# Kernel tuning notes

Hardware: AMD Instinct MI355X
Metric: run time of the kernel (lower is better)

The kernel has to match this reference:

```python
import jax, jax.numpy as jnp
import numpy as np

N = 8192          # number of nodes
DIN = 512         # in_features
DOUT = 256        # out_features
P_EDGE = 0.004    # ~32 avg degree
NEG_INF = -9e15   # matches the torch module's -9000000000000000.0 mask value


def setup_inputs() -> dict:
    key = jax.random.key(0)
    ks = jax.random.split(key, 7)
    x = jax.random.normal(ks[0], (N, DIN), dtype=jnp.float32)
    # binary adjacency, Bernoulli(P_EDGE)
    adj = (jax.random.uniform(ks[1], (N, N)) < P_EDGE).astype(jnp.float32)
    W1 = jax.random.normal(ks[2], (DIN, DOUT), dtype=jnp.float32) * 0.05
    b1 = jnp.zeros((DOUT,), dtype=jnp.float32)
    a1_w = jax.random.normal(ks[3], (DOUT,), dtype=jnp.float32) * 0.05
    a1_b = jnp.zeros((), dtype=jnp.float32)
    a2_w = jax.random.normal(ks[4], (DOUT,), dtype=jnp.float32) * 0.05
    a2_b = jnp.zeros((), dtype=jnp.float32)
    return {"x": x, "adj": adj, "W1": W1, "b1": b1,
            "a1_w": a1_w, "a1_b": a1_b, "a2_w": a2_w, "a2_b": a2_b}


def reference(x, adj, W1, b1, a1_w, a1_b, a2_w, a2_b):
    # h = linear1(elu(x))                       [n, DOUT]
    h = jnp.matmul(jax.nn.elu(x), W1) + b1
    # per-node scalar scores g1 (source/col) and g2 (dest/row)
    g1 = h @ a1_w + a1_b                       # [n]
    g2 = h @ a2_w + a2_b                       # [n]
    # kron trick collapses to: scores[i,j] = adj[i,j] * (g2[i] + g1[j])
    scores = adj * (g2[:, None] + g1[None, :])  # [n, n]
    e = jax.nn.leaky_relu(scores, negative_slope=0.2)
    attention = jax.nn.softmax(jnp.where(adj > 0, e, NEG_INF), axis=1)
    # untied=False path: weighted aggregation of h (dropout p=0 is identity)
    return attention @ h
```

## Files before the change

### kernel.cpp

```cpp
#include <hip/hip_runtime.h>
#include <hip/hip_bf16.h>
#include <cstdint>
#include <cstddef>

#define N_NODES 8192
#define DIN 512
#define DOUT 256
#define CAP 512

typedef short bf16x8 __attribute__((ext_vector_type(8)));
typedef float f32x4 __attribute__((ext_vector_type(4)));
typedef unsigned int u32x4 __attribute__((ext_vector_type(4)));

__device__ __forceinline__ float bf2f(unsigned short u) {
    union { unsigned int ui; float f; } v; v.ui = ((unsigned int)u) << 16; return v.f;
}
__device__ __forceinline__ unsigned short f2bf(float f) {
    union { float f; unsigned int u; } v; v.f = f;
    unsigned int u = v.u;
    return (unsigned short)((u + 0x7fffu + ((u >> 16) & 1u)) >> 16);
}
__device__ __forceinline__ float elu1(float v) { return v > 0.f ? v : (expf(v) - 1.f); }

__global__ __launch_bounds__(256) void gemm_h_kernel(
    const float* __restrict__ x, const float* __restrict__ W1,
    const float* __restrict__ b1, unsigned short* __restrict__ h)
{
    const int tid = threadIdx.x;
    const int wave = tid >> 6, lane = tid & 63;
    const int quad = lane >> 4, r16 = lane & 15;
    const int m0 = (blockIdx.x >> 2) * 64;
    const int col = (blockIdx.x & 3) * 64 + wave * 16 + r16;

    f32x4 acc[4] = {{0.f,0.f,0.f,0.f},{0.f,0.f,0.f,0.f},{0.f,0.f,0.f,0.f},{0.f,0.f,0.f,0.f}};

    for (int k0 = 0; k0 < DIN; k0 += 32) {
        const int kbase = k0 + quad * 8;
        bf16x8 bfr;
        #pragma unroll
        for (int j = 0; j < 8; ++j)
            bfr[j] = (short)f2bf(W1[(size_t)(kbase + j) * DOUT + col]);
        #pragma unroll
        for (int r = 0; r < 4; ++r) {
            const float* xrow = x + (size_t)(m0 + r * 16 + r16) * DIN;
            float4 f0 = *(const float4*)(xrow + kbase);
            float4 f1 = *(const float4*)(xrow + kbase + 4);
            bf16x8 af;
            af[0] = (short)f2bf(elu1(f0.x)); af[1] = (short)f2bf(elu1(f0.y));
            af[2] = (short)f2bf(elu1(f0.z)); af[3] = (short)f2bf(elu1(f0.w));
            af[4] = (short)f2bf(elu1(f1.x)); af[5] = (short)f2bf(elu1(f1.y));
            af[6] = (short)f2bf(elu1(f1.z)); af[7] = (short)f2bf(elu1(f1.w));
            acc[r] = __builtin_amdgcn_mfma_f32_16x16x32_bf16(af, bfr, acc[r], 0, 0, 0);
        }
    }
    const float bias = b1[col];
    #pragma unroll
    for (int r = 0; r < 4; ++r)
        #pragma unroll
        for (int rr = 0; rr < 4; ++rr)
            h[(size_t)(m0 + r * 16 + quad * 4 + rr) * DOUT + col] = f2bf(acc[r][rr] + bias);
}

__global__ __launch_bounds__(256) void g12_kernel(
    const unsigned short* __restrict__ h,
    const float* __restrict__ a1w, const float* __restrict__ a1b,
    const float* __restrict__ a2w, const float* __restrict__ a2b,
    float* __restrict__ g1, float* __restrict__ g2)
{
    const int tid = threadIdx.x;
    const int wave = tid >> 6, lane = tid & 63;
    const int i = blockIdx.x * 4 + wave;
    const int d0 = lane * 4;
    ushort4 hv = *(const ushort4*)(h + (size_t)i * DOUT + d0);
    float4 w1 = *(const float4*)(a1w + d0);
    float4 w2 = *(const float4*)(a2w + d0);
    float h0 = bf2f(hv.x), h1 = bf2f(hv.y), h2 = bf2f(hv.z), h3 = bf2f(hv.w);
    float s1 = h0*w1.x + h1*w1.y + h2*w1.z + h3*w1.w;
    float s2 = h0*w2.x + h1*w2.y + h2*w2.z + h3*w2.w;
    #pragma unroll
    for (int off = 32; off > 0; off >>= 1) {
        s1 += __shfl_xor(s1, off, 64);
        s2 += __shfl_xor(s2, off, 64);
    }
    if (lane == 0) {
        g1[i] = s1 + a1b[0];
        g2[i] = s2 + a2b[0];
    }
}

__global__ __launch_bounds__(256) void scan_kernel(
    const float* __restrict__ adj, const float* __restrict__ g1,
    const float* __restrict__ g2,
    int* __restrict__ ej, float* __restrict__ evg, int* __restrict__ cnts)
{
    __shared__ int   eidx[CAP];
    __shared__ float ev[CAP];
    __shared__ int   cnt;

    const int tid = threadIdx.x;
    const int i = blockIdx.x;
    if (tid == 0) cnt = 0;
    __syncthreads();

    const float g2i = g2[i];
    const float* arow = adj + (size_t)i * N_NODES;

    u32x4 raws[8];
    #pragma unroll
    for (int c = 0; c < 8; ++c)
        raws[c] = __builtin_nontemporal_load((const u32x4*)(arow + c * 1024 + tid * 4));

    #pragma unroll
    for (int c = 0; c < 8; ++c) {
        u32x4 raw = raws[c];
        if (raw.x | raw.y | raw.z | raw.w) {
            unsigned int wv[4] = {raw.x, raw.y, raw.z, raw.w};
            #pragma unroll
            for (int q = 0; q < 4; ++q) {
                if (wv[q]) {
                    int j = c * 1024 + tid * 4 + q;
                    union { unsigned int u; float f; } av; av.u = wv[q];
                    float s = av.f * (g2i + g1[j]);
                    float lr = s > 0.f ? s : 0.2f * s;
                    int pos = atomicAdd(&cnt, 1);
                    if (pos < CAP) { eidx[pos] = j; ev[pos] = lr; }
                }
            }
        }
    }
    __syncthreads();
    const int K = cnt < CAP ? cnt : CAP;
    for (int k = tid; k < K; k += 256) {
        ej[(size_t)i * CAP + k]  = eidx[k];
        evg[(size_t)i * CAP + k] = ev[k];
    }
    if (tid == 0) cnts[i] = K;
}

__global__ __launch_bounds__(256) void finish_kernel(
    const int* __restrict__ ej, const float* __restrict__ evg,
    const int* __restrict__ cnts, const unsigned short* __restrict__ h,
    float* __restrict__ out)
{
    __shared__ int   jbuf[CAP];
    __shared__ float pbuf[CAP];
    __shared__ float sinv;

    const int tid = threadIdx.x;
    const int i = blockIdx.x;
    const int K = cnts[i];

    if (K == 0) {
        float acc = 0.f;
        for (int j = 0; j < N_NODES; ++j) acc += bf2f(h[(size_t)j * DOUT + tid]);
        out[(size_t)i * DOUT + tid] = acc / (float)N_NODES;
        return;
    }

    for (int k = tid; k < K; k += 256) {
        jbuf[k] = ej[(size_t)i * CAP + k];
        pbuf[k] = evg[(size_t)i * CAP + k];
    }
    __syncthreads();

    if (tid < 64) {
        const int lane = tid;
        float mloc = -1e30f;
        for (int k = lane; k < K; k += 64) mloc = fmaxf(mloc, pbuf[k]);
        #pragma unroll
        for (int off = 32; off > 0; off >>= 1) mloc = fmaxf(mloc, __shfl_xor(mloc, off, 64));
        float sloc = 0.f;
        for (int k = lane; k < K; k += 64) { float p = expf(pbuf[k] - mloc); pbuf[k] = p; sloc += p; }
        #pragma unroll
        for (int off = 32; off > 0; off >>= 1) sloc += __shfl_xor(sloc, off, 64);
        if (lane == 0) sinv = 1.f / sloc;
    }
    __syncthreads();
    const float inv = sinv;

    float acc = 0.f;
    int k = 0;
    for (; k + 4 <= K; k += 4) {
        float p0 = pbuf[k],   p1 = pbuf[k+1], p2 = pbuf[k+2], p3 = pbuf[k+3];
        int   j0 = jbuf[k],   j1 = jbuf[k+1], j2 = jbuf[k+2], j3 = jbuf[k+3];
        float v0 = bf2f(h[(size_t)j0 * DOUT + tid]);
        float v1 = bf2f(h[(size_t)j1 * DOUT + tid]);
        float v2 = bf2f(h[(size_t)j2 * DOUT + tid]);
        float v3 = bf2f(h[(size_t)j3 * DOUT + tid]);
        acc += p0 * v0 + p1 * v1 + p2 * v2 + p3 * v3;
    }
    for (; k < K; ++k) acc += pbuf[k] * bf2f(h[(size_t)jbuf[k] * DOUT + tid]);
    out[(size_t)i * DOUT + tid] = acc * inv;
}

extern "C" void kernel_launch(void* const* d_in, const int* in_sizes, int n_in,
                              void* d_out, int out_size, void* d_ws, size_t ws_size,
                              hipStream_t stream) {
    const float* x   = (const float*)d_in[0];
    const float* adj = (const float*)d_in[1];
    const float* W1  = (const float*)d_in[2];
    const float* b1  = (const float*)d_in[3];
    const float* a1w = (const float*)d_in[4];
    const float* a1b = (const float*)d_in[5];
    const float* a2w = (const float*)d_in[6];
    const float* a2b = (const float*)d_in[7];

    char* w = (char*)d_ws;
    float* g1 = (float*)w;                                   w += (size_t)N_NODES * 4;
    float* g2 = (float*)w;                                   w += (size_t)N_NODES * 4;
    unsigned short* h = (unsigned short*)w;                  w += (size_t)N_NODES * DOUT * 2;
    int* ej = (int*)w;                                       w += (size_t)N_NODES * CAP * 4;
    float* evg = (float*)w;                                  w += (size_t)N_NODES * CAP * 4;
    int* cnts = (int*)w;
    float* out = (float*)d_out;

    hipLaunchKernelGGL(gemm_h_kernel,  dim3(512),  dim3(256), 0, stream, x, W1, b1, h);
    hipLaunchKernelGGL(g12_kernel,     dim3(2048), dim3(256), 0, stream, h, a1w, a1b, a2w, a2b, g1, g2);
    hipLaunchKernelGGL(scan_kernel,    dim3(8192), dim3(256), 0, stream, adj, g1, g2, ej, evg, cnts);
    hipLaunchKernelGGL(finish_kernel,  dim3(8192), dim3(256), 0, stream, ej, evg, cnts, h, out);
}
```

Baseline: 427.0 us.

## Flatten adjacency scan into grid-stride pass with global atomics; compute scores in finish

The scan no longer assigns one block per row. It now sweeps the whole adjacency matrix with a grid-stride loop of coalesced 16-byte loads, and appends column indices per row through global atomics on a per-row counter. A new kernel zeroes those counters first. Edge scores are no longer computed and stored in the scan; finish recomputes leaky_relu(g2[i]+g1[j]) from the gathered indices, which drops the evg buffer traffic and the shared-memory staging and block syncs in the scan. The change assumes adjacency values are exactly 1 and makes edge order, and so summation order, nondeterministic.

```diff
diff --git a/kernel.cpp b/kernel.cpp
--- a/kernel.cpp
+++ b/kernel.cpp
@@ -7,6 +7,7 @@
 #define DIN 512
 #define DOUT 256
 #define CAP 512
+#define NCHUNK (N_NODES * N_NODES / 4)
 
 typedef short bf16x8 __attribute__((ext_vector_type(8)));
 typedef float f32x4 __attribute__((ext_vector_type(4)));
@@ -21,6 +22,10 @@
     return (unsigned short)((u + 0x7fffu + ((u >> 16) & 1u)) >> 16);
 }
 __device__ __forceinline__ float elu1(float v) { return v > 0.f ? v : (expf(v) - 1.f); }
+
+__global__ __launch_bounds__(256) void zero_cnts_kernel(int* __restrict__ cnts) {
+    cnts[blockIdx.x * 256 + threadIdx.x] = 0;
+}
 
 __global__ __launch_bounds__(256) void gemm_h_kernel(
     const float* __restrict__ x, const float* __restrict__ W1,
@@ -89,58 +94,41 @@
 }
 
 __global__ __launch_bounds__(256) void scan_kernel(
-    const float* __restrict__ adj, const float* __restrict__ g1,
-    const float* __restrict__ g2,
-    int* __restrict__ ej, float* __restrict__ evg, int* __restrict__ cnts)
-{
-    __shared__ int   eidx[CAP];
-    __shared__ float ev[CAP];
-    __shared__ int   cnt;
-
-    const int tid = threadIdx.x;
-    const int i = blockIdx.x;
-    if (tid == 0) cnt = 0;
-    __syncthreads();
-
-    const float g2i = g2[i];
-    const float* arow = adj + (size_t)i * N_NODES;
-
-    u32x4 raws[8];
-    #pragma unroll
-    for (int c = 0; c < 8; ++c)
-        raws[c] = __builtin_nontemporal_load((const u32x4*)(arow + c * 1024 + tid * 4));
-
-    #pragma unroll
-    for (int c = 0; c < 8; ++c) {
-        u32x4 raw = raws[c];
-        if (raw.x | raw.y | raw.z | raw.w) {
-            unsigned int wv[4] = {raw.x, raw.y, raw.z, raw.w};
-            #pragma unroll
-            for (int q = 0; q < 4; ++q) {
-                if (wv[q]) {
-                    int j = c * 1024 + tid * 4 + q;
-                    union { unsigned int u; float f; } av; av.u = wv[q];
-                    float s = av.f * (g2i + g1[j]);
-                    float lr = s > 0.f ? s : 0.2f * s;
-                    int pos = atomicAdd(&cnt, 1);
-                    if (pos < CAP) { eidx[pos] = j; ev[pos] = lr; }
+    const u32x4* __restrict__ adj4, int* __restrict__ ej, int* __restrict__ cnts)
+{
+    const int gtid = blockIdx.x * 256 + threadIdx.x;
+    const int stride = gridDim.x * 256;
+    for (int it = 0; it < 16; it += 4) {
+        u32x4 r[4];
+        int cidx[4];
+        #pragma unroll
+        for (int u = 0; u < 4; ++u) {
+            cidx[u] = gtid + (it + u) * stride;
+            r[u] = adj4[cidx[u]];
+        }
+        #pragma unroll
+        for (int u = 0; u < 4; ++u) {
+            if (r[u].x | r[u].y | r[u].z | r[u].w) {
+                const int elem = cidx[u] * 4;
+                const int row = elem >> 13;
+                const int col0 = elem & 8191;
+                unsigned int wv[4] = {r[u].x, r[u].y, r[u].z, r[u].w};
+                #pragma unroll
+                for (int q = 0; q < 4; ++q) {
+                    if (wv[q]) {
+                        int pos = atomicAdd(&cnts[row], 1);
+                        if (pos < CAP) ej[(size_t)row * CAP + pos] = col0 + q;
+                    }
                 }
             }
         }
     }
-    __syncthreads();
-    const int K = cnt < CAP ? cnt : CAP;
-    for (int k = tid; k < K; k += 256) {
-        ej[(size_t)i * CAP + k]  = eidx[k];
-        evg[(size_t)i * CAP + k] = ev[k];
-    }
-    if (tid == 0) cnts[i] = K;
 }
 
 __global__ __launch_bounds__(256) void finish_kernel(
-    const int* __restrict__ ej, const float* __restrict__ evg,
-    const int* __restrict__ cnts, const unsigned short* __restrict__ h,
-    float* __restrict__ out)
+    const int* __restrict__ ej, const int* __restrict__ cnts,
+    const float* __restrict__ g1, const float* __restrict__ g2,
+    const unsigned short* __restrict__ h, float* __restrict__ out)
 {
     __shared__ int   jbuf[CAP];
     __shared__ float pbuf[CAP];
@@ -148,7 +136,7 @@
 
     const int tid = threadIdx.x;
     const int i = blockIdx.x;
-    const int K = cnts[i];
+    int K = cnts[i]; if (K > CAP) K = CAP;
 
     if (K == 0) {
         float acc = 0.f;
@@ -157,16 +145,19 @@
         return;
     }
 
-    for (int k = tid; k < K; k += 256) {
-        jbuf[k] = ej[(size_t)i * CAP + k];
-        pbuf[k] = evg[(size_t)i * CAP + k];
-    }
+    for (int k = tid; k < K; k += 256) jbuf[k] = ej[(size_t)i * CAP + k];
     __syncthreads();
 
     if (tid < 64) {
         const int lane = tid;
+        const float g2i = g2[i];
         float mloc = -1e30f;
-        for (int k = lane; k < K; k += 64) mloc = fmaxf(mloc, pbuf[k]);
+        for (int k = lane; k < K; k += 64) {
+            float s = g2i + g1[jbuf[k]];
+            float lr = s > 0.f ? s : 0.2f * s;
+            pbuf[k] = lr;
+            mloc = fmaxf(mloc, lr);
+        }
         #pragma unroll
         for (int off = 32; off > 0; off >>= 1) mloc = fmaxf(mloc, __shfl_xor(mloc, off, 64));
         float sloc = 0.f;
@@ -206,16 +197,16 @@
     const float* a2b = (const float*)d_in[7];
 
     char* w = (char*)d_ws;
-    float* g1 = (float*)w;                                   w += (size_t)N_NODES * 4;
-    float* g2 = (float*)w;                                   w += (size_t)N_NODES * 4;
-    unsigned short* h = (unsigned short*)w;                  w += (size_t)N_NODES * DOUT * 2;
-    int* ej = (int*)w;                                       w += (size_t)N_NODES * CAP * 4;
-    float* evg = (float*)w;                                  w += (size_t)N_NODES * CAP * 4;
+    float* g1 = (float*)w;                    w += (size_t)N_NODES * 4;
+    float* g2 = (float*)w;                    w += (size_t)N_NODES * 4;
+    unsigned short* h = (unsigned short*)w;   w += (size_t)N_NODES * DOUT * 2;
+    int* ej = (int*)w;                        w += (size_t)N_NODES * CAP * 4;
     int* cnts = (int*)w;
     float* out = (float*)d_out;
 
-    hipLaunchKernelGGL(gemm_h_kernel,  dim3(512),  dim3(256), 0, stream, x, W1, b1, h);
-    hipLaunchKernelGGL(g12_kernel,     dim3(2048), dim3(256), 0, stream, h, a1w, a1b, a2w, a2b, g1, g2);
-    hipLaunchKernelGGL(scan_kernel,    dim3(8192), dim3(256), 0, stream, adj, g1, g2, ej, evg, cnts);
-    hipLaunchKernelGGL(finish_kernel,  dim3(8192), dim3(256), 0, stream, ej, evg, cnts, h, out);
-}
+    hipLaunchKernelGGL(zero_cnts_kernel, dim3(32),   dim3(256), 0, stream, cnts);
+    hipLaunchKernelGGL(gemm_h_kernel,    dim3(512),  dim3(256), 0, stream, x, W1, b1, h);
+    hipLaunchKernelGGL(g12_kernel,       dim3(2048), dim3(256), 0, stream, h, a1w, a1b, a2w, a2b, g1, g2);
+    hipLaunchKernelGGL(scan_kernel,      dim3(4096), dim3(256), 0, stream, (const u32x4*)adj, ej, cnts);
+    hipLaunchKernelGGL(finish_kernel,    dim3(8192), dim3(256), 0, stream, ej, cnts, g1, g2, h, out);
+}
```

Result: slower. 469.8 us (+10.0%).
